# Kernel tuning notes

Measured on AMD Instinct MI355X. Metric: run time of the kernel, lower is better.

## Reference

```python
import jax, jax.numpy as jnp
import numpy as np

FP8_MAX = 448.0  # max finite value of float8_e4m3fn


def _fp8_quant(v, scale):
    # emulate saturating scaled cast to float8_e4m3fn, then dequant-free fp8 storage (upcast to f32 for the gemm)
    q = jnp.clip(v / scale, -FP8_MAX, FP8_MAX)
    return q.astype(jnp.float8_e4m3fn).astype(jnp.float32)


def setup_inputs() -> dict:
    key = jax.random.key(0)
    k0, k1, k2, k3 = jax.random.split(key, 4)
    T, H, I, E = 1024, 1024, 2816, 8
    x = jax.random.normal(k0, (T, H), jnp.float32)
    router_logits = jax.random.normal(k1, (T, E), jnp.float32)
    w13_weight = jax.random.normal(k2, (E, 2 * I, H), jnp.float32) * 0.02
    w2_weight = jax.random.normal(k3, (E, H, I), jnp.float32) * 0.02
    return {
        "x": x,
        "router_logits": router_logits,
        "w13_weight": w13_weight,
        "w2_weight": w2_weight,
        "w13_input_scale": jnp.ones((E,), jnp.float32),
        "w2_input_scale": jnp.ones((E,), jnp.float32),
        "top_k": 2,
    }


def reference(x, router_logits, w13_weight, w2_weight, w13_input_scale, w2_input_scale, top_k):
    T, H = x.shape
    E, two_I, _ = w13_weight.shape
    I = two_I // 2

    # --- routing: softmax -> top_k -> renormalize (select_experts) ---
    probs = jax.nn.softmax(router_logits, axis=-1)
    topk_w, topk_ids = jax.lax.top_k(probs, top_k)            # [T,K]
    topk_w = topk_w / jnp.sum(topk_w, axis=-1, keepdims=True)
    # dense combine matrix [T,E]: sparsity of the grouped gemm dispatch
    combine = jnp.zeros((T, E), x.dtype).at[jnp.arange(T)[:, None], topk_ids].add(topk_w)

    # --- per-expert fp8 weight quantization (ops.scaled_fp8_quant per expert) ---
    w13_scale = jnp.max(jnp.abs(w13_weight), axis=(1, 2)) / FP8_MAX  # [E]
    w2_scale = jnp.max(jnp.abs(w2_weight), axis=(1, 2)) / FP8_MAX
    w13_q = _fp8_quant(w13_weight, w13_scale[:, None, None])         # [E,2I,H]
    w2_q = _fp8_quant(w2_weight, w2_scale[:, None, None])            # [E,H,I]

    # --- grouped gemm 1: per-expert activation quant + fp8 gemm + dequant scale ---
    x_q = _fp8_quant(x[None], w13_input_scale[:, None, None])        # [E,T,H]
    h = jnp.einsum('eth,eih->eti', x_q, w13_q) * (w13_input_scale * w13_scale)[:, None, None]

    # --- silu_and_mul: gate = first intermediate_size rows, up = second ---
    act = jax.nn.silu(h[..., :I]) * h[..., I:]                       # [E,T,I]

    # --- grouped gemm 2 ---
    act_q = _fp8_quant(act, w2_input_scale[:, None, None])
    o = jnp.einsum('eti,ehi->eth', act_q, w2_q) * (w2_input_scale * w2_scale)[:, None, None]

    # --- post_reorder: weighted combine of selected experts ---
    return jnp.einsum('te,eth->th', combine, o)                      # [T,H]
```

## Files before the change

### kernel.cpp

```cpp
#include <hip/hip_runtime.h>
#include <cstdint>
#include <cstddef>

#define T_TOK 1024
#define H_DIM 1024
#define I_DIM 2816
#define E_NUM 8
#define PAIRS 2048
#define KSPLIT 4
#define NT1 88
#define AMX2_X 32

typedef __attribute__((ext_vector_type(4))) float f32x4;
typedef __attribute__((ext_vector_type(4))) unsigned int u32x4;
typedef long i64;

__device__ __forceinline__ unsigned char fp8e4m3_sw(float v) {
  v = fminf(448.f, fmaxf(-448.f, v));
  unsigned b = __float_as_uint(v);
  unsigned s = (b >> 24) & 0x80u;
  float a = fabsf(v);
  if (a < 0.015625f) {
    int m = (int)rintf(a * 512.f);
    return (unsigned char)(s | (unsigned)m);
  }
  unsigned ab = b & 0x7fffffffu;
  unsigned rnd = 0x7FFFFu + ((ab >> 20) & 1u);
  ab += rnd;
  int e = (int)(ab >> 23) - 127;
  unsigned m = (ab >> 20) & 7u;
  if (e > 8 || (e == 8 && m > 6)) { e = 8; m = 6; }
  return (unsigned char)(s | (unsigned)((e + 7) << 3) | m);
}

__device__ __forceinline__ unsigned q4(float a, float b, float c, float d) {
#if __has_builtin(__builtin_amdgcn_cvt_pk_fp8_f32)
  unsigned w = (unsigned)__builtin_amdgcn_cvt_pk_fp8_f32(a, b, 0, false);
  return (unsigned)__builtin_amdgcn_cvt_pk_fp8_f32(c, d, (int)w, true);
#else
  return (unsigned)fp8e4m3_sw(a) | ((unsigned)fp8e4m3_sw(b) << 8) |
         ((unsigned)fp8e4m3_sw(c) << 16) | ((unsigned)fp8e4m3_sw(d) << 24);
#endif
}

__device__ __forceinline__ unsigned char q1(float a) {
#if __has_builtin(__builtin_amdgcn_cvt_pk_fp8_f32)
  return (unsigned char)((unsigned)__builtin_amdgcn_cvt_pk_fp8_f32(a, a, 0, false) & 0xFFu);
#else
  return fp8e4m3_sw(a);
#endif
}

__device__ __forceinline__ unsigned q4v(float4 f, float inv) {
  return q4(f.x * inv, f.y * inv, f.z * inv, f.w * inv);
}

__device__ __forceinline__ unsigned q4c(float4 f, float inv) {
  float a = fminf(448.f, fmaxf(-448.f, f.x * inv));
  float b = fminf(448.f, fmaxf(-448.f, f.y * inv));
  float c = fminf(448.f, fmaxf(-448.f, f.z * inv));
  float d = fminf(448.f, fmaxf(-448.f, f.w * inv));
  return q4(a, b, c, d);
}

__device__ __forceinline__ float wave_max(float m) {
#pragma unroll
  for (int off = 32; off > 0; off >>= 1) m = fmaxf(m, __shfl_xor(m, off));
  return m;
}

__device__ __forceinline__ void top2(const float* l, int& i0, int& i1) {
  i0 = 0; float b0 = l[0];
#pragma unroll
  for (int k = 1; k < E_NUM; k++) { if (l[k] > b0) { b0 = l[k]; i0 = k; } }
  i1 = -1; float b1 = -3.4e38f;
#pragma unroll
  for (int k = 0; k < E_NUM; k++) { if (k != i0 && l[k] > b1) { b1 = l[k]; i1 = k; } }
}

__global__ __launch_bounds__(256) void pre_k(const float* __restrict__ w13,
                                             const float* __restrict__ logits,
                                             const float* __restrict__ x,
                                             const float* __restrict__ s13,
                                             float* __restrict__ part13,
                                             int* __restrict__ cnt_g,
                                             int* __restrict__ offs_g,
                                             int* __restrict__ pair_xrow,
                                             float* __restrict__ pair_w,
                                             int* __restrict__ pairidx,
                                             unsigned char* __restrict__ Xq) {
  const int tid = threadIdx.x;
  if (blockIdx.x < 1024) {
    const int e = blockIdx.x >> 7, sub = blockIdx.x & 127;
    const float4* src = (const float4*)w13 + (size_t)e * (2 * I_DIM * H_DIM / 4);
    int idx = sub * 256 + tid;
    const int stride = 128 * 256;
    float m = 0.f;
#pragma unroll
    for (int j = 0; j < 44; j += 4) {
      float4 v0 = src[idx + (size_t)(j + 0) * stride];
      float4 v1 = src[idx + (size_t)(j + 1) * stride];
      float4 v2 = src[idx + (size_t)(j + 2) * stride];
      float4 v3 = src[idx + (size_t)(j + 3) * stride];
      m = fmaxf(m, fmaxf(fmaxf(fabsf(v0.x), fabsf(v0.y)), fmaxf(fabsf(v0.z), fabsf(v0.w))));
      m = fmaxf(m, fmaxf(fmaxf(fabsf(v1.x), fabsf(v1.y)), fmaxf(fabsf(v1.z), fabsf(v1.w))));
      m = fmaxf(m, fmaxf(fmaxf(fabsf(v2.x), fabsf(v2.y)), fmaxf(fabsf(v2.z), fabsf(v2.w))));
      m = fmaxf(m, fmaxf(fmaxf(fabsf(v3.x), fabsf(v3.y)), fmaxf(fabsf(v3.z), fabsf(v3.w))));
    }
    m = wave_max(m);
    __shared__ float wmax[4];
    int lane = tid & 63, wid = tid >> 6;
    if (lane == 0) wmax[wid] = m;
    __syncthreads();
    if (tid == 0)
      part13[blockIdx.x] = fmaxf(fmaxf(wmax[0], wmax[1]), fmaxf(wmax[2], wmax[3]));
    return;
  }

  if (blockIdx.x == 1024) {
    __shared__ int cnt_s[E_NUM], pos_s[E_NUM];
    if (tid < E_NUM) cnt_s[tid] = 0;
    __syncthreads();
    int i0s[4], i1s[4];
    float w0s[4], w1s[4];
#pragma unroll
    for (int j = 0; j < 4; j++) {
      int t = tid * 4 + j;
      float l[E_NUM];
#pragma unroll
      for (int k = 0; k < E_NUM; k++) l[k] = logits[t * E_NUM + k];
      int i0, i1;
      top2(l, i0, i1);
      float e1 = expf(l[i1] - l[i0]);
      float d = 1.f + e1;
      i0s[j] = i0; i1s[j] = i1; w0s[j] = 1.f / d; w1s[j] = e1 / d;
      atomicAdd(&cnt_s[i0], 1);
      atomicAdd(&cnt_s[i1], 1);
    }
    __syncthreads();
    if (tid == 0) {
      int s = 0;
#pragma unroll
      for (int e = 0; e < E_NUM; e++) {
        cnt_g[e] = cnt_s[e];
        offs_g[e] = s;
        pos_s[e] = s;
        s += cnt_s[e];
      }
      offs_g[E_NUM] = s;
    }
    __syncthreads();
#pragma unroll
    for (int j = 0; j < 4; j++) {
      int t = tid * 4 + j;
      int s0 = atomicAdd(&pos_s[i0s[j]], 1);
      pair_xrow[s0] = 2 * t; pair_w[s0] = w0s[j]; pairidx[2 * t] = s0;
      int s1 = atomicAdd(&pos_s[i1s[j]], 1);
      pair_xrow[s1] = 2 * t + 1; pair_w[s1] = w1s[j]; pairidx[2 * t + 1] = s1;
    }
    return;
  }

  {
    const int q = blockIdx.x - 1025;
#pragma unroll
    for (int j = 0; j < 2; j++) {
      int t = q * 2 + j;
      float l[E_NUM];
#pragma unroll
      for (int k = 0; k < E_NUM; k++) l[k] = logits[t * E_NUM + k];
      int i0, i1;
      top2(l, i0, i1);
      float inv0 = 1.f / s13[i0];
      float inv1 = 1.f / s13[i1];
      float4 v = ((const float4*)(x + (size_t)t * H_DIM))[tid];
      ((unsigned*)(Xq + (size_t)(2 * t) * H_DIM))[tid] = q4c(v, inv0);
      ((unsigned*)(Xq + (size_t)(2 * t + 1) * H_DIM))[tid] = q4c(v, inv1);
    }
  }
}

__global__ __launch_bounds__(512) void gemm1_k(const float* __restrict__ w13,
                                               const float* __restrict__ w2,
                                               const unsigned char* __restrict__ Xq,
                                               unsigned char* __restrict__ H1,
                                               const int* __restrict__ cnt,
                                               const int* __restrict__ offs,
                                               const float* __restrict__ part13,
                                               float* __restrict__ part2,
                                               const int* __restrict__ pair_xrow,
                                               const float* __restrict__ s13,
                                               const float* __restrict__ s2in) {
  const int e = blockIdx.z;
  const int tid = threadIdx.x, lane = tid & 63, wq = tid >> 6;

  if (blockIdx.x >= NT1) {
    const int bx2 = (blockIdx.x - NT1) * 4 + blockIdx.y;
    const float4* src = (const float4*)w2 + (size_t)e * (H_DIM * I_DIM / 4);
    int idx = bx2 * 512 + tid;
    const int stride = 128 * 512;
    float m = 0.f;
#pragma unroll
    for (int j = 0; j < 11; j++) {
      float4 v = src[idx + (size_t)j * stride];
      m = fmaxf(m, fmaxf(fmaxf(fabsf(v.x), fabsf(v.y)), fmaxf(fabsf(v.z), fabsf(v.w))));
    }
    m = wave_max(m);
    __shared__ float wmax2[8];
    if (lane == 0) wmax2[wq] = m;
    __syncthreads();
    if (tid == 0) {
      float mm = wmax2[0];
#pragma unroll
      for (int j = 1; j < 8; j++) mm = fmaxf(mm, wmax2[j]);
      part2[e * 128 + bx2] = mm;
    }
    return;
  }

  __shared__ float redA[8];
  {
    float v = part13[e * 128 + (tid & 127)];
    v = wave_max(v);
    if (lane == 0) redA[wq] = v;
  }
  __syncthreads();
  float amax = redA[0];
#pragma unroll
  for (int j = 1; j < 8; j++) amax = fmaxf(amax, redA[j]);

  const int count = cnt[e];
  const int m0 = blockIdx.y * 256;
  if (m0 >= count) return;
  const int nt = blockIdx.x;
  const int base = offs[e];

  const float inv_w = 448.f / amax;
  const float gs = s13[e] * (amax / 448.f);
  const float inv_a2 = 1.f / s2in[e];

  __shared__ __align__(16) unsigned char As[2][256][80];
  __shared__ __align__(16) unsigned char Bs[2][64][80];

  const int fr = lane & 15, ks = lane >> 4;

  f32x4 accg[2][2], accu[2][2];
#pragma unroll
  for (int i = 0; i < 2; i++)
#pragma unroll
    for (int j = 0; j < 2; j++) { accg[i][j] = (f32x4)0.f; accu[i][j] = (f32x4)0.f; }

  const int ar0 = tid >> 2, aseg = tid & 3;
  int pr0 = base + m0 + ar0;       if (pr0 > PAIRS - 1) pr0 = PAIRS - 1;
  int pr1 = base + m0 + ar0 + 128; if (pr1 > PAIRS - 1) pr1 = PAIRS - 1;
  const unsigned char* a_src0 = Xq + (size_t)pair_xrow[pr0] * H_DIM + aseg * 16;
  const unsigned char* a_src1 = Xq + (size_t)pair_xrow[pr1] * H_DIM + aseg * 16;

  const int brow = tid >> 3, bseg = tid & 7;
  const size_t brg = (size_t)nt * 32 + (brow & 31) + (size_t)(brow >> 5) * I_DIM;
  const float* b_src = w13 + ((size_t)e * 2 * I_DIM + brg) * H_DIM + bseg * 8;

  const int NIT = H_DIM / 64;

  u32x4 ra0 = *(const u32x4*)a_src0;
  u32x4 ra1 = *(const u32x4*)a_src1;
  float4 fb0 = ((const float4*)b_src)[0], fb1 = ((const float4*)b_src)[1];
  {
    unsigned q0 = q4v(fb0, inv_w), q1_ = q4v(fb1, inv_w);
    *(u32x4*)&As[0][ar0][aseg * 16] = ra0;
    *(u32x4*)&As[0][ar0 + 128][aseg * 16] = ra1;
    ((unsigned*)&Bs[0][brow][bseg * 8])[0] = q0;
    ((unsigned*)&Bs[0][brow][bseg * 8])[1] = q1_;
  }
  ra0 = *(const u32x4*)(a_src0 + 64);
  ra1 = *(const u32x4*)(a_src1 + 64);
  fb0 = ((const float4*)(b_src + 64))[0];
  fb1 = ((const float4*)(b_src + 64))[1];
  unsigned qb0 = q4v(fb0, inv_w), qb1 = q4v(fb1, inv_w);
  __syncthreads();

  int c = 0;
  for (int t = 0; t < NIT; ++t) {
    if (t + 1 < NIT) {
      *(u32x4*)&As[c ^ 1][ar0][aseg * 16] = ra0;
      *(u32x4*)&As[c ^ 1][ar0 + 128][aseg * 16] = ra1;
      ((unsigned*)&Bs[c ^ 1][brow][bseg * 8])[0] = qb0;
      ((unsigned*)&Bs[c ^ 1][brow][bseg * 8])[1] = qb1;
    }
    if (t + 2 < NIT) {
      int k0 = (t + 2) * 64;
      ra0 = *(const u32x4*)(a_src0 + k0);
      ra1 = *(const u32x4*)(a_src1 + k0);
      fb0 = ((const float4*)(b_src + k0))[0];
      fb1 = ((const float4*)(b_src + k0))[1];
    }
#pragma unroll
    for (int kk = 0; kk < 2; kk++) {
      i64 a0 = *(const i64*)&As[c][wq * 32 + fr][kk * 32 + ks * 8];
      i64 a1 = *(const i64*)&As[c][wq * 32 + 16 + fr][kk * 32 + ks * 8];
#pragma unroll
      for (int ni = 0; ni < 2; ni++) {
        i64 bg = *(const i64*)&Bs[c][ni * 16 + fr][kk * 32 + ks * 8];
        i64 bu = *(const i64*)&Bs[c][32 + ni * 16 + fr][kk * 32 + ks * 8];
        accg[0][ni] = __builtin_amdgcn_mfma_f32_16x16x32_fp8_fp8(a0, bg, accg[0][ni], 0, 0, 0);
        accg[1][ni] = __builtin_amdgcn_mfma_f32_16x16x32_fp8_fp8(a1, bg, accg[1][ni], 0, 0, 0);
        accu[0][ni] = __builtin_amdgcn_mfma_f32_16x16x32_fp8_fp8(a0, bu, accu[0][ni], 0, 0, 0);
        accu[1][ni] = __builtin_amdgcn_mfma_f32_16x16x32_fp8_fp8(a1, bu, accu[1][ni], 0, 0, 0);
      }
    }
    if (t + 2 < NIT) {
      qb0 = q4v(fb0, inv_w);
      qb1 = q4v(fb1, inv_w);
    }
    __syncthreads();
    c ^= 1;
  }

  const int rg = lane >> 4;
#pragma unroll
  for (int mi = 0; mi < 2; mi++) {
#pragma unroll
    for (int rr = 0; rr < 4; rr++) {
      int lrow = wq * 32 + mi * 16 + rg * 4 + rr;
      if (m0 + lrow < count) {
        size_t p = (size_t)(base + m0 + lrow);
#pragma unroll
        for (int ni = 0; ni < 2; ni++) {
          int col = nt * 32 + ni * 16 + fr;
          float g = accg[mi][ni][rr] * gs;
          float u = accu[mi][ni][rr] * gs;
          float act = g / (1.f + expf(-g)) * u * inv_a2;
          act = fminf(448.f, fmaxf(-448.f, act));
          H1[p * I_DIM + col] = q1(act);
        }
      }
    }
  }
}

__global__ __launch_bounds__(512) void gemm2_k(const float* __restrict__ w2,
                                               const unsigned char* __restrict__ H1,
                                               float* __restrict__ Op,
                                               const int* __restrict__ cnt,
                                               const int* __restrict__ offs,
                                               const float* __restrict__ part2,
                                               const float* __restrict__ s2in,
                                               const float* __restrict__ pair_w) {
  const int e = blockIdx.z;
  const int tid = threadIdx.x, lane = tid & 63, wq = tid >> 6;

  __shared__ float redA[8];
  {
    float v = part2[e * 128 + (tid & 127)];
    v = wave_max(v);
    if (lane == 0) redA[wq] = v;
  }
  __syncthreads();
  float amax = redA[0];
#pragma unroll
  for (int j = 1; j < 8; j++) amax = fmaxf(amax, redA[j]);

  const int count = cnt[e];
  const int m0 = blockIdx.y * 128;
  if (m0 >= count) return;
  const int nt = blockIdx.x & 15;
  const int ksp = blockIdx.x >> 4;
  const int n0 = nt * 64;
  const int base = offs[e];

  const float inv_w = 448.f / amax;
  const float s2 = s2in[e] * (amax / 448.f);

  __shared__ __align__(16) unsigned char As[2][128][80];
  __shared__ __align__(16) unsigned char Bs[2][64][80];

  const int fr = lane & 15, ks = lane >> 4;

  f32x4 acc[4];
#pragma unroll
  for (int i = 0; i < 4; i++) acc[i] = (f32x4)0.f;

  const int arow = tid >> 2, aseg = tid & 3;
  int pr = base + m0 + arow; if (pr > PAIRS - 1) pr = PAIRS - 1;
  const unsigned char* a_src = H1 + (size_t)pr * I_DIM + aseg * 16;

  const int brow = tid >> 3, bseg = tid & 7;
  const float* b_src = w2 + ((size_t)e * H_DIM + n0 + brow) * I_DIM + bseg * 8;

  const int KITER = (I_DIM / 64) / KSPLIT;
  const int kbase = ksp * KITER * 64;

  u32x4 ra = *(const u32x4*)(a_src + kbase);
  float4 fb0 = ((const float4*)(b_src + kbase))[0];
  float4 fb1 = ((const float4*)(b_src + kbase))[1];
  {
    unsigned q0 = q4v(fb0, inv_w), q1_ = q4v(fb1, inv_w);
    *(u32x4*)&As[0][arow][aseg * 16] = ra;
    ((unsigned*)&Bs[0][brow][bseg * 8])[0] = q0;
    ((unsigned*)&Bs[0][brow][bseg * 8])[1] = q1_;
  }
  ra = *(const u32x4*)(a_src + kbase + 64);
  fb0 = ((const float4*)(b_src + kbase + 64))[0];
  fb1 = ((const float4*)(b_src + kbase + 64))[1];
  unsigned qb0 = q4v(fb0, inv_w), qb1 = q4v(fb1, inv_w);
  __syncthreads();

  int c = 0;
  for (int t = 0; t < KITER; ++t) {
    if (t + 1 < KITER) {
      *(u32x4*)&As[c ^ 1][arow][aseg * 16] = ra;
      ((unsigned*)&Bs[c ^ 1][brow][bseg * 8])[0] = qb0;
      ((unsigned*)&Bs[c ^ 1][brow][bseg * 8])[1] = qb1;
    }
    if (t + 2 < KITER) {
      int k0 = kbase + (t + 2) * 64;
      ra = *(const u32x4*)(a_src + k0);
      fb0 = ((const float4*)(b_src + k0))[0];
      fb1 = ((const float4*)(b_src + k0))[1];
    }
#pragma unroll
    for (int kk = 0; kk < 2; kk++) {
      i64 a0 = *(const i64*)&As[c][wq * 16 + fr][kk * 32 + ks * 8];
#pragma unroll
      for (int ni = 0; ni < 4; ni++) {
        i64 b = *(const i64*)&Bs[c][ni * 16 + fr][kk * 32 + ks * 8];
        acc[ni] = __builtin_amdgcn_mfma_f32_16x16x32_fp8_fp8(a0, b, acc[ni], 0, 0, 0);
      }
    }
    if (t + 2 < KITER) {
      qb0 = q4v(fb0, inv_w);
      qb1 = q4v(fb1, inv_w);
    }
    __syncthreads();
    c ^= 1;
  }

  const int rg = lane >> 4;
#pragma unroll
  for (int rr = 0; rr < 4; rr++) {
    int lrow = wq * 16 + rg * 4 + rr;
    if (m0 + lrow < count) {
      size_t p = (size_t)(base + m0 + lrow);
      float pw = pair_w[p];
#pragma unroll
      for (int ni = 0; ni < 4; ni++) {
        int col = n0 + ni * 16 + fr;
        Op[((size_t)ksp * PAIRS + p) * H_DIM + col] = acc[ni][rr] * s2 * pw;
      }
    }
  }
}

__global__ __launch_bounds__(256) void combine_k(const float* __restrict__ Op,
                                                 const int* __restrict__ pairidx,
                                                 float* __restrict__ out) {
  int t = blockIdx.x;
  int p0 = pairidx[2 * t], p1 = pairidx[2 * t + 1];
  f32x4 acc = (f32x4)0.f;
#pragma unroll
  for (int s = 0; s < KSPLIT; s++) {
    f32x4 a = ((const f32x4*)(Op + ((size_t)s * PAIRS + p0) * H_DIM))[threadIdx.x];
    f32x4 b = ((const f32x4*)(Op + ((size_t)s * PAIRS + p1) * H_DIM))[threadIdx.x];
    acc += a + b;
  }
  ((f32x4*)(out + (size_t)t * H_DIM))[threadIdx.x] = acc;
}

extern "C" void kernel_launch(void* const* d_in, const int* in_sizes, int n_in,
                              void* d_out, int out_size, void* d_ws, size_t ws_size,
                              hipStream_t stream) {
  (void)in_sizes; (void)n_in; (void)out_size; (void)ws_size;
  const float* x      = (const float*)d_in[0];
  const float* logits = (const float*)d_in[1];
  const float* w13    = (const float*)d_in[2];
  const float* w2     = (const float*)d_in[3];
  const float* s13    = (const float*)d_in[4];
  const float* s2in   = (const float*)d_in[5];
  float* out = (float*)d_out;

  char* ws = (char*)d_ws;
  int* cnt       = (int*)(ws + 128);
  int* offs      = (int*)(ws + 192);
  float* part13  = (float*)(ws + 4096);
  float* part2   = (float*)(ws + 8192);
  int* pair_xrow = (int*)(ws + 17408);
  float* pair_w  = (float*)(ws + 25600);
  int* pairidx   = (int*)(ws + 33792);
  unsigned char* Xq = (unsigned char*)(ws + (size_t)(1 << 20));
  unsigned char* H1 = (unsigned char*)(ws + (size_t)4 * (1 << 20));
  float* Op         = (float*)(ws + (size_t)10 * (1 << 20));

  pre_k<<<1537, 256, 0, stream>>>(w13, logits, x, s13, part13, cnt, offs,
                                  pair_xrow, pair_w, pairidx, Xq);

  gemm1_k<<<dim3(NT1 + AMX2_X, 4, E_NUM), 512, 0, stream>>>(
      w13, w2, Xq, H1, cnt, offs, part13, part2, pair_xrow, s13, s2in);

  gemm2_k<<<dim3(16 * KSPLIT, 8, E_NUM), 512, 0, stream>>>(
      w2, H1, Op, cnt, offs, part2, s2in, pair_w);

  combine_k<<<T_TOK, 256, 0, stream>>>(Op, pairidx, out);
}
```

Baseline: 163.7 us.

## Pre-quantize w13 to fp8 in a separate kernel before gemm1

Adds a quantw13_k kernel that converts the fp32 w13 weights to fp8 once per expert, using the amax already reduced in part13, and stores them in workspace. gemm1 then streams 8-byte fp8 B tiles instead of 32-byte fp32 ones and drops the in-loop quantization. The aim is to avoid re-reading fp32 weights and re-quantizing them for every active M-tile block, and to lighten gemm1's inner loop. The cost is an extra launch plus writing and re-reading a 46MB fp8 buffer, which must go through L2/MALL or HBM.

```diff
diff --git a/kernel.cpp b/kernel.cpp
--- a/kernel.cpp
+++ b/kernel.cpp
@@ -13,6 +13,7 @@
 
 typedef __attribute__((ext_vector_type(4))) float f32x4;
 typedef __attribute__((ext_vector_type(4))) unsigned int u32x4;
+typedef __attribute__((ext_vector_type(2))) unsigned int u32x2;
 typedef long i64;
 
 __device__ __forceinline__ unsigned char fp8e4m3_sw(float v) {
@@ -180,7 +181,33 @@
   }
 }
 
-__global__ __launch_bounds__(512) void gemm1_k(const float* __restrict__ w13,
+__global__ __launch_bounds__(256) void quantw13_k(const float* __restrict__ w13,
+                                                  const float* __restrict__ part13,
+                                                  unsigned char* __restrict__ Wq13) {
+  const int e = blockIdx.y;
+  const int tid = threadIdx.x, lane = tid & 63, wq = tid >> 6;
+  __shared__ float redA[4];
+  {
+    float v = part13[e * 128 + (tid & 127)];
+    v = wave_max(v);
+    if (lane == 0) redA[wq] = v;
+  }
+  __syncthreads();
+  float amax = fmaxf(fmaxf(redA[0], redA[1]), fmaxf(redA[2], redA[3]));
+  const float inv_w = 448.f / amax;
+
+  const float4* src = (const float4*)w13 + (size_t)e * (2 * I_DIM * H_DIM / 4);
+  unsigned* dst = (unsigned*)(Wq13 + (size_t)e * 2 * I_DIM * H_DIM);
+  int idx = blockIdx.x * 256 + tid;
+  const int stride = 176 * 256;
+#pragma unroll
+  for (int j = 0; j < 32; j++) {
+    float4 f = src[idx + (size_t)j * stride];
+    dst[idx + (size_t)j * stride] = q4v(f, inv_w);
+  }
+}
+
+__global__ __launch_bounds__(512) void gemm1_k(const unsigned char* __restrict__ Wq13,
                                                const float* __restrict__ w2,
                                                const unsigned char* __restrict__ Xq,
                                                unsigned char* __restrict__ H1,
@@ -235,7 +262,6 @@
   const int nt = blockIdx.x;
   const int base = offs[e];
 
-  const float inv_w = 448.f / amax;
   const float gs = s13[e] * (amax / 448.f);
   const float inv_a2 = 1.f / s2in[e];
 
@@ -258,25 +284,22 @@
 
   const int brow = tid >> 3, bseg = tid & 7;
   const size_t brg = (size_t)nt * 32 + (brow & 31) + (size_t)(brow >> 5) * I_DIM;
-  const float* b_src = w13 + ((size_t)e * 2 * I_DIM + brg) * H_DIM + bseg * 8;
+  const unsigned char* b_src = Wq13 + ((size_t)e * 2 * I_DIM + brg) * H_DIM + bseg * 8;
 
   const int NIT = H_DIM / 64;
 
   u32x4 ra0 = *(const u32x4*)a_src0;
   u32x4 ra1 = *(const u32x4*)a_src1;
-  float4 fb0 = ((const float4*)b_src)[0], fb1 = ((const float4*)b_src)[1];
+  u32x2 rb = *(const u32x2*)b_src;
   {
-    unsigned q0 = q4v(fb0, inv_w), q1_ = q4v(fb1, inv_w);
     *(u32x4*)&As[0][ar0][aseg * 16] = ra0;
     *(u32x4*)&As[0][ar0 + 128][aseg * 16] = ra1;
-    ((unsigned*)&Bs[0][brow][bseg * 8])[0] = q0;
-    ((unsigned*)&Bs[0][brow][bseg * 8])[1] = q1_;
+    ((unsigned*)&Bs[0][brow][bseg * 8])[0] = rb.x;
+    ((unsigned*)&Bs[0][brow][bseg * 8])[1] = rb.y;
   }
   ra0 = *(const u32x4*)(a_src0 + 64);
   ra1 = *(const u32x4*)(a_src1 + 64);
-  fb0 = ((const float4*)(b_src + 64))[0];
-  fb1 = ((const float4*)(b_src + 64))[1];
-  unsigned qb0 = q4v(fb0, inv_w), qb1 = q4v(fb1, inv_w);
+  rb = *(const u32x2*)(b_src + 64);
   __syncthreads();
 
   int c = 0;
@@ -284,15 +307,14 @@
     if (t + 1 < NIT) {
       *(u32x4*)&As[c ^ 1][ar0][aseg * 16] = ra0;
       *(u32x4*)&As[c ^ 1][ar0 + 128][aseg * 16] = ra1;
-      ((unsigned*)&Bs[c ^ 1][brow][bseg * 8])[0] = qb0;
-      ((unsigned*)&Bs[c ^ 1][brow][bseg * 8])[1] = qb1;
+      ((unsigned*)&Bs[c ^ 1][brow][bseg * 8])[0] = rb.x;
+      ((unsigned*)&Bs[c ^ 1][brow][bseg * 8])[1] = rb.y;
     }
     if (t + 2 < NIT) {
       int k0 = (t + 2) * 64;
       ra0 = *(const u32x4*)(a_src0 + k0);
       ra1 = *(const u32x4*)(a_src1 + k0);
-      fb0 = ((const float4*)(b_src + k0))[0];
-      fb1 = ((const float4*)(b_src + k0))[1];
+      rb = *(const u32x2*)(b_src + k0);
     }
 #pragma unroll
     for (int kk = 0; kk < 2; kk++) {
@@ -307,10 +329,6 @@
         accu[0][ni] = __builtin_amdgcn_mfma_f32_16x16x32_fp8_fp8(a0, bu, accu[0][ni], 0, 0, 0);
         accu[1][ni] = __builtin_amdgcn_mfma_f32_16x16x32_fp8_fp8(a1, bu, accu[1][ni], 0, 0, 0);
       }
-    }
-    if (t + 2 < NIT) {
-      qb0 = q4v(fb0, inv_w);
-      qb1 = q4v(fb1, inv_w);
     }
     __syncthreads();
     c ^= 1;
@@ -489,12 +507,15 @@
   unsigned char* Xq = (unsigned char*)(ws + (size_t)(1 << 20));
   unsigned char* H1 = (unsigned char*)(ws + (size_t)4 * (1 << 20));
   float* Op         = (float*)(ws + (size_t)10 * (1 << 20));
+  unsigned char* Wq13 = (unsigned char*)(ws + (size_t)48 * (1 << 20));
 
   pre_k<<<1537, 256, 0, stream>>>(w13, logits, x, s13, part13, cnt, offs,
                                   pair_xrow, pair_w, pairidx, Xq);
 
+  quantw13_k<<<dim3(176, E_NUM), 256, 0, stream>>>(w13, part13, Wq13);
+
   gemm1_k<<<dim3(NT1 + AMX2_X, 4, E_NUM), 512, 0, stream>>>(
-      w13, w2, Xq, H1, cnt, offs, part13, part2, pair_xrow, s13, s2in);
+      Wq13, w2, Xq, H1, cnt, offs, part13, part2, pair_xrow, s13, s2in);
 
   gemm2_k<<<dim3(16 * KSPLIT, 8, E_NUM), 512, 0, stream>>>(
       w2, H1, Op, cnt, offs, part2, s2in, pair_w);
```

After: 180.3 us. 10.1% more time.
